# Kernel tuning notes

Measured on AMD Instinct MI355X. Metric: run time of the kernel, lower is better.

Reference implementation:

```python
import jax, jax.numpy as jnp
import numpy as np

N, E, B = 50000, 800000, 64
F0, H, C = 8, 2, 64          # node feat dim, heads, per-head out dim
OBS, MH, NA = 128, 256, 16   # obs dim, mlp hidden, n_actions
NEG_SLOPE = 0.2


def setup_inputs() -> dict:
    key = jax.random.key(0)
    ks = jax.random.split(key, 30)
    p = lambda k, shape: (jax.random.normal(k, shape, dtype=jnp.float32) * 0.1)
    inp = {
        "obs": jax.random.normal(ks[0], (B, OBS), dtype=jnp.float32),
        "node_features": jax.random.normal(ks[1], (N, F0), dtype=jnp.float32),
        "edge_index": jax.random.randint(ks[2], (2, E), 0, N, dtype=jnp.int32),
        "batch": jnp.sort(jax.random.randint(ks[3], (N,), 0, B, dtype=jnp.int32)),
        # GAT layer 0: in=F0 -> heads=H, out=C, concat
        "W0": p(ks[4], (F0, H * C)), "a_src0": p(ks[5], (H, C)), "a_dst0": p(ks[6], (H, C)), "b0": p(ks[7], (H * C,)),
        # GAT layer 1: in=H*C -> heads=H, out=C, concat
        "W1": p(ks[8], (H * C, H * C)), "a_src1": p(ks[9], (H, C)), "a_dst1": p(ks[10], (H, C)), "b1": p(ks[11], (H * C,)),
        # GAT layer 2: in=H*C -> heads=1, out=C, no concat
        "W2": p(ks[12], (H * C, C)), "a_src2": p(ks[13], (1, C)), "a_dst2": p(ks[14], (1, C)), "b2": p(ks[15], (C,)),
        # MLP head: combined = C + OBS
        "Ws1": p(ks[16], (C + OBS, MH)), "bs1": p(ks[17], (MH,)),
        "ln_g": jnp.ones((MH,), jnp.float32), "ln_b": jnp.zeros((MH,), jnp.float32),
        "Ws2": p(ks[18], (MH, MH)), "bs2": p(ks[19], (MH,)),
        "Wa": p(ks[20], (MH, NA)), "ba": p(ks[21], (NA,)),
        "Wc": p(ks[22], (MH, 1)), "bc": p(ks[23], (1,)),
    }
    return inp


def gat_layer(x, src, dst, W, a_src, a_dst, bias, heads, out_dim, concat):
    n = x.shape[0]
    h = (x @ W).reshape(n, heads, out_dim)                     # [N,H,C]
    alpha_s = jnp.einsum("nhc,hc->nh", h, a_src)               # [N,H]
    alpha_d = jnp.einsum("nhc,hc->nh", h, a_dst)
    e = jax.nn.leaky_relu(alpha_s[src] + alpha_d[dst], NEG_SLOPE)  # [E,H]
    # scatter-softmax over incoming edges of each dst node (stable)
    emax = jax.ops.segment_max(e, dst, num_segments=n)
    ex = jnp.exp(e - emax[dst])
    denom = jax.ops.segment_sum(ex, dst, num_segments=n)
    alpha = ex / (denom[dst] + 1e-16)                          # [E,H]
    msg = h[src] * alpha[..., None]                            # [E,H,C]
    out = jax.ops.segment_sum(msg, dst, num_segments=n)        # [N,H,C]
    out = out.reshape(n, heads * out_dim) if concat else out.mean(axis=1)
    return out + bias


def reference(obs, node_features, edge_index, batch,
              W0, a_src0, a_dst0, b0, W1, a_src1, a_dst1, b1,
              W2, a_src2, a_dst2, b2,
              Ws1, bs1, ln_g, ln_b, Ws2, bs2, Wa, ba, Wc, bc):
    n = node_features.shape[0]
    # PyG GATConv default add_self_loops=True
    loop = jnp.arange(n, dtype=edge_index.dtype)
    src = jnp.concatenate([edge_index[0], loop])
    dst = jnp.concatenate([edge_index[1], loop])

    x = node_features
    x = jax.nn.elu(gat_layer(x, src, dst, W0, a_src0, a_dst0, b0, H, C, True))
    x = jax.nn.elu(gat_layer(x, src, dst, W1, a_src1, a_dst1, b1, H, C, True))
    x = gat_layer(x, src, dst, W2, a_src2, a_dst2, b2, 1, C, False)

    # global mean pool over graphs
    counts = jax.ops.segment_sum(jnp.ones((n,), x.dtype), batch, num_segments=B)
    pooled = jax.ops.segment_sum(x, batch, num_segments=B) / jnp.maximum(counts, 1.0)[:, None]

    combined = jnp.concatenate([pooled, obs], axis=-1)         # [B, C+OBS]
    h = combined @ Ws1 + bs1
    mu = h.mean(-1, keepdims=True)
    var = ((h - mu) ** 2).mean(-1, keepdims=True)
    h = (h - mu) / jnp.sqrt(var + 1e-5) * ln_g + ln_b
    h = jax.nn.relu(h)
    h = jax.nn.relu(h @ Ws2 + bs2)
    logits = h @ Wa + ba
    value = (h @ Wc + bc).squeeze(-1)
    return logits, value
```

## Files before the change

### kernel.cpp

```cpp
#include <hip/hip_runtime.h>
#include <math.h>


#define LRELU(x) ((x) > 0.f ? (x) : 0.2f * (x))

typedef short bf16x8 __attribute__((ext_vector_type(8)));
typedef unsigned short u16x8 __attribute__((ext_vector_type(8)));
typedef float f32x4 __attribute__((ext_vector_type(4)));
typedef float f32x2 __attribute__((ext_vector_type(2)));

__device__ __forceinline__ unsigned short f2bf(float f) {
    unsigned int u = __float_as_uint(f);
    u = (u + 0x7fffu + ((u >> 16) & 1u)) >> 16;
    return (unsigned short)u;
}
__device__ __forceinline__ float bf2f(unsigned short u) {
    return __uint_as_float((unsigned int)u << 16);
}
__device__ __forceinline__ unsigned char f2fp8(float f) {
    return (unsigned char)(__builtin_amdgcn_cvt_pk_fp8_f32(f, f, 0, false) & 0xff);
}
__device__ __forceinline__ f32x2 fp8pair(unsigned int u) {
    return __builtin_amdgcn_cvt_pk_f32_fp8(u, false);
}


__global__ __launch_bounds__(256) void hist_t0_kernel(
    const int* __restrict__ dst, int* __restrict__ histT,
    int e, int G1, int NB, int n, int hist_blocks, int t0_blocks, int wp_blocks,
    const float* __restrict__ x, const float* __restrict__ W,
    const float* __restrict__ a_src, const float* __restrict__ a_dst,
    unsigned char* __restrict__ h, float* __restrict__ as_o,
    float* __restrict__ ad_o,
    const float* __restrict__ W1, const float* __restrict__ W2,
    unsigned short* __restrict__ Wf1, unsigned short* __restrict__ Wf2,
    const int* __restrict__ batch, int* __restrict__ gstart, int nGraphs) {
    __shared__ unsigned int hist[512];
    __shared__ float xs[2][8][8];
    const int t = threadIdx.x;
    if ((int)blockIdx.x < hist_blocks) {
        hist[t] = 0;
        hist[t + 256] = 0;
        __syncthreads();
        const int g = blockIdx.x;
#pragma unroll
        for (int jj = 0; jj < 8; jj++) {
            int idx = g * 8192 + jj * 1024 + t * 4;
            int d[4];
            if (idx + 4 <= e) {
                int4 dd = *(const int4*)(dst + idx);
                d[0] = dd.x; d[1] = dd.y; d[2] = dd.z; d[3] = dd.w;
            } else {
#pragma unroll
                for (int q = 0; q < 4; q++) d[q] = (idx + q < e) ? dst[idx + q] : -1;
            }
#pragma unroll
            for (int q = 0; q < 4; q++)
                if (d[q] >= 0) atomicAdd(&hist[d[q] >> 7], 1u);
        }
        __syncthreads();
        if (t < NB) histT[g * NB + t] = (int)hist[t];
        if (t + 256 < NB) histT[g * NB + t + 256] = (int)hist[t + 256];
        return;
    }
    if ((int)blockIdx.x < hist_blocks + t0_blocks) {
        const int bid2 = blockIdx.x - hist_blocks;
        const int tid = t & 127;
        const int half = t >> 7;
        const int node0 = bid2 * 16 + half * 8;

        for (int idx = tid; idx < 64; idx += 128) {
            int ni = idx >> 3, k = idx & 7;
            int ng = node0 + ni;
            xs[half][ni][k] = (ng < n) ? x[(size_t)ng * 8 + k] : 0.f;
        }
        __syncthreads();

        float acc[8];
#pragma unroll
        for (int i = 0; i < 8; i++) acc[i] = 0.f;
#pragma unroll
        for (int k = 0; k < 8; k++) {
            float wk = W[k * 128 + tid];
#pragma unroll
            for (int i = 0; i < 8; i++) acc[i] += xs[half][i][k] * wk;
        }

        const int lane = tid & 63;
        const int head = tid >> 6;
        const int pos = 2 * lane + head;
        const float av = a_src[tid];
        const float dv = a_dst[tid];
#pragma unroll
        for (int i = 0; i < 8; i++) {
            int ng = node0 + i;
            if (ng >= n) break;
            h[(size_t)ng * 128 + pos] = f2fp8(acc[i]);
            float ps = acc[i] * av, pd = acc[i] * dv;
            for (int off = 32; off; off >>= 1) {
                ps += __shfl_xor(ps, off, 64);
                pd += __shfl_xor(pd, off, 64);
            }
            if (lane == 0) {
                as_o[ng * 2 + head] = ps;
                ad_o[ng * 2 + head] = pd;
            }
        }
        return;
    }
    if ((int)blockIdx.x < hist_blocks + t0_blocks + wp_blocks) {
        const int n1 = 8 * 4 * 64;
        const int n2 = 4 * 4 * 64;
        int gid = (blockIdx.x - hist_blocks - t0_blocks) * 256 + t;
        if (gid < n1) {
            int idx = gid;
            int lane = idx & 63, ts = idx >> 6;
            int s = ts & 3, tt = ts >> 2;
            int quad = lane >> 4, cn = lane & 15;
#pragma unroll
            for (int j = 0; j < 8; j++)
                Wf1[idx * 8 + j] = f2bf(W1[(s * 32 + quad * 8 + j) * 128 + tt * 16 + cn]);
        } else if (gid < n1 + n2) {
            int idx = gid - n1;
            int lane = idx & 63, ts = idx >> 6;
            int s = ts & 3, tt = ts >> 2;
            int quad = lane >> 4, cn = lane & 15;
#pragma unroll
            for (int j = 0; j < 8; j++)
                Wf2[idx * 8 + j] = f2bf(W2[(s * 32 + quad * 8 + j) * 64 + tt * 16 + cn]);
        }
        return;
    }
    int gid = (blockIdx.x - hist_blocks - t0_blocks - wp_blocks) * 256 + t;
    if (gid < n) {
        int bi = batch[gid];
        if (gid == 0) {
            for (int g = 0; g <= bi; g++) gstart[g] = 0;
        } else {
            int bp = batch[gid - 1];
            if (bi != bp)
                for (int g = bp + 1; g <= bi; g++) gstart[g] = gid;
        }
        if (gid == n - 1) {
            for (int g = bi + 1; g <= nGraphs; g++) gstart[g] = n;
        }
    }
}


__global__ __launch_bounds__(256) void bucket_scatter_kernel(
    const int* __restrict__ src, const int* __restrict__ dst,
    const int* __restrict__ histT, int* __restrict__ esrc,
    unsigned char* __restrict__ dsub8, int* __restrict__ prefA,
    int e, int G1, int NB) {
    __shared__ int totL[512], scn[256], prefL[512], baseL[512];
    __shared__ unsigned cnt[512];
    const int t = threadIdx.x;
    const int g = blockIdx.x;

    int p0 = 0, tt0 = 0, p1 = 0, tt1 = 0;
    const bool hasHi = (t + 256) < NB;
    for (int g2 = 0; g2 < G1; g2++) {
        int v0 = (t < NB) ? histT[g2 * NB + t] : 0;
        int v1 = hasHi ? histT[g2 * NB + t + 256] : 0;
        if (g2 < g) { p0 += v0; p1 += v1; }
        tt0 += v0; tt1 += v1;
    }
    totL[t] = (t < NB) ? tt0 : 0;
    totL[t + 256] = hasHi ? tt1 : 0;
    __syncthreads();
    int v0 = totL[2 * t], v1 = totL[2 * t + 1];
    int s = v0 + v1;
    scn[t] = s;
    __syncthreads();
    for (int off = 1; off < 256; off <<= 1) {
        int u = (t >= off) ? scn[t - off] : 0;
        __syncthreads();
        scn[t] += u;
        __syncthreads();
    }
    int base2 = scn[t] - s;
    prefL[2 * t] = base2;
    prefL[2 * t + 1] = base2 + v0;
    __syncthreads();
    baseL[t] = prefL[t] + p0;
    baseL[t + 256] = prefL[t + 256] + p1;
    cnt[t] = 0;
    cnt[t + 256] = 0;
    if (g == 0) {
        if (t < NB) prefA[t] = prefL[t];
        if (hasHi) prefA[t + 256] = prefL[t + 256];
        if (t == 0) prefA[NB] = scn[255];
    }
    __syncthreads();

#pragma unroll
    for (int jj = 0; jj < 8; jj++) {
        int idx = g * 8192 + jj * 1024 + t * 4;
        int d[4], sv[4];
        if (idx + 4 <= e) {
            int4 dd = *(const int4*)(dst + idx);
            int4 ss = *(const int4*)(src + idx);
            d[0] = dd.x; d[1] = dd.y; d[2] = dd.z; d[3] = dd.w;
            sv[0] = ss.x; sv[1] = ss.y; sv[2] = ss.z; sv[3] = ss.w;
        } else {
#pragma unroll
            for (int q = 0; q < 4; q++) {
                bool v = idx + q < e;
                d[q] = v ? dst[idx + q] : -1;
                sv[q] = v ? src[idx + q] : 0;
            }
        }
        unsigned r[4];
#pragma unroll
        for (int q = 0; q < 4; q++)
            r[q] = (d[q] >= 0) ? atomicAdd(&cnt[d[q] >> 7], 1u) : 0u;
#pragma unroll
        for (int q = 0; q < 4; q++) {
            if (d[q] >= 0) {
                int pos = baseL[d[q] >> 7] + (int)r[q];
                esrc[pos] = sv[q];
                dsub8[pos] = (unsigned char)(d[q] & 127);
            }
        }
    }
}


__global__ __launch_bounds__(256) void bucket_csr_kernel(
    const int* __restrict__ prefA, const unsigned char* __restrict__ dsub8,
    const int* __restrict__ esrc, int* __restrict__ row_ptr,
    int* __restrict__ col, int n) {
    __shared__ unsigned int cnt[128];
    __shared__ int rp[128];
    const int t = threadIdx.x;
    const int b = blockIdx.x;
    const int bs = prefA[b];
    const int be = prefA[b + 1];
    if (t < 128) cnt[t] = 0;
    __syncthreads();
    for (int i = bs + t; i < be; i += 256) {
        atomicAdd(&cnt[dsub8[i]], 1u);
    }
    __syncthreads();
    int v = 0;
    if (t < 128) { v = (int)cnt[t]; rp[t] = v; }
    __syncthreads();
    for (int off = 1; off < 128; off <<= 1) {
        int u = (t >= off && t < 128) ? rp[t - off] : 0;
        __syncthreads();
        if (t < 128) rp[t] += u;
        __syncthreads();
    }
    if (t < 128) {
        int excl = rp[t] - v;
        int node = b * 128 + t;
        if (node <= n) row_ptr[node] = bs + excl;
        cnt[t] = (unsigned)excl;
    }
    __syncthreads();
    for (int i = bs + t; i < be; i += 256) {
        int sub = dsub8[i];
        unsigned r = atomicAdd(&cnt[sub], 1u);
        col[bs + (int)r] = esrc[i];
    }
}

template <int OUT, int HEADS>
__device__ __forceinline__ int hpos8(int c) {
    return (HEADS == 2) ? (2 * (c & 63) + (c >> 6)) : c;
}


template <int OUT, int HEADS>
__global__ __launch_bounds__(256) void transform_mfma_kernel(
    const unsigned short* __restrict__ xb, const unsigned short* __restrict__ Wf,
    const float* __restrict__ a_src, const float* __restrict__ a_dst,
    unsigned char* __restrict__ h, float* __restrict__ as_o, float* __restrict__ ad_o,
    int n) {
    constexpr int T = OUT / 16, S = 4;
    const int w = threadIdx.x >> 6, lane = threadIdx.x & 63;
    const int node0 = (blockIdx.x * 4 + w) * 16;
    if (node0 >= n) return;
    const int quad = lane >> 4, col = lane & 15;

    const int arow = node0 + col;
    const bool aok = arow < n;
    bf16x8 a[S];
    const unsigned short* xrow = xb + (size_t)arow * 128 + quad * 8;
#pragma unroll
    for (int s = 0; s < S; s++) {
        bf16x8 z = {0, 0, 0, 0, 0, 0, 0, 0};
        a[s] = aok ? *(const bf16x8*)(xrow + s * 32) : z;
    }

    f32x4 acc[T];
#pragma unroll
    for (int t = 0; t < T; t++) acc[t] = (f32x4){0.f, 0.f, 0.f, 0.f};

#pragma unroll
    for (int s = 0; s < S; s++) {
#pragma unroll
        for (int t = 0; t < T; t++) {
            bf16x8 b = *(const bf16x8*)(Wf + ((size_t)(t * S + s) * 64 + lane) * 8);
            acc[t] = __builtin_amdgcn_mfma_f32_16x16x32_bf16(a[s], b, acc[t], 0, 0, 0);
        }
    }

#pragma unroll
    for (int t = 0; t < T; t++) {
        int pos = hpos8<OUT, HEADS>(t * 16 + col);
#pragma unroll
        for (int r = 0; r < 4; r++) {
            int m = node0 + quad * 4 + r;
            if (m < n) h[(size_t)m * OUT + pos] = f2fp8(acc[t][r]);
        }
    }

#pragma unroll
    for (int r = 0; r < 4; r++) {
        float s0 = 0.f, s1 = 0.f, d0 = 0.f, d1 = 0.f;
#pragma unroll
        for (int t = 0; t < T; t++) {
            float av = a_src[t * 16 + col];
            float dv = a_dst[t * 16 + col];
            float v = acc[t][r];
            if (HEADS == 2 && t >= T / 2) { s1 += v * av; d1 += v * dv; }
            else                          { s0 += v * av; d0 += v * dv; }
        }
        for (int off = 8; off; off >>= 1) {
            s0 += __shfl_xor(s0, off, 64);
            d0 += __shfl_xor(d0, off, 64);
            if (HEADS == 2) {
                s1 += __shfl_xor(s1, off, 64);
                d1 += __shfl_xor(d1, off, 64);
            }
        }
        int m = node0 + quad * 4 + r;
        if (m < n) {
            if (HEADS == 2) {
                if (col == 0)      { as_o[m * 2] = s0;     ad_o[m * 2] = d0; }
                else if (col == 1) { as_o[m * 2 + 1] = s1; ad_o[m * 2 + 1] = d1; }
            } else {
                if (col == 0) { as_o[m] = s0; ad_o[m] = d0; }
            }
        }
    }
}


template <int ACT>
__global__ __launch_bounds__(256) void agg2_kernel(
    const int* __restrict__ row_ptr, const int* __restrict__ col,
    const unsigned char* __restrict__ h, const float2* __restrict__ as2,
    const float2* __restrict__ ad2, const float* __restrict__ bias,
    unsigned short* __restrict__ out, int n) {
    __shared__ float w0l[4][2][32], w1l[4][2][32];
    __shared__ unsigned sofl[4][2][32];
    const int w = threadIdx.x >> 6;
    const int lane = threadIdx.x & 63;
    const int half = lane >> 5, l = lane & 31;
    const int node = blockIdx.x * 8 + w * 2 + half;
    const bool active = node < n;

    int beg = 0, deg = 0;
    float2 adv = make_float2(0.f, 0.f);
    float den0 = 0.f, den1 = 0.f;
    float a0 = 0.f, a1 = 0.f, a2 = 0.f, a3 = 0.f;
    if (active) {
        beg = row_ptr[node];
        deg = row_ptr[node + 1] - beg;
        adv = ad2[node];
        float2 avs = as2[node];
        float w0s = __expf(LRELU(avs.x + adv.x));
        float w1s = __expf(LRELU(avs.y + adv.y));
        unsigned us = *(const unsigned*)(h + ((size_t)node << 7) + 4 * l);
        f32x2 p0 = fp8pair(us & 0xffffu);
        f32x2 p1 = fp8pair(us >> 16);
        a0 = w0s * p0.x; a1 = w1s * p0.y;
        a2 = w0s * p1.x; a3 = w1s * p1.y;
        den0 = w0s; den1 = w1s;
    }
    int dmax = deg;
    for (int off = 32; off; off >>= 1) dmax = max(dmax, __shfl_xor(dmax, off, 64));

    for (int base = 0; base < dmax; base += 32) {
        int cnt = deg - base;
        cnt = cnt < 0 ? 0 : (cnt > 32 ? 32 : cnt);
        float w0 = 0.f, w1 = 0.f;
        unsigned so = 0;
        if (l < cnt) {
            int s = col[beg + base + l];
            float2 av = as2[s];
            w0 = __expf(LRELU(av.x + adv.x));
            w1 = __expf(LRELU(av.y + adv.y));
            so = (unsigned)s << 7;
        }
        float t0 = w0, t1 = w1;
        for (int off = 16; off; off >>= 1) {
            t0 += __shfl_xor(t0, off, 64);
            t1 += __shfl_xor(t1, off, 64);
        }
        den0 += t0; den1 += t1;
        w0l[w][half][l] = w0;
        w1l[w][half][l] = w1;
        sofl[w][half][l] = so;

        int jmax = dmax - base;
        jmax = jmax > 32 ? 32 : jmax;
        for (int j = 0; j < jmax; j += 8) {
            unsigned u[8];
#pragma unroll
            for (int k = 0; k < 8; k++) {
                unsigned so_k = sofl[w][half][j + k];
                u[k] = *(const unsigned*)(h + so_k + 4 * l);
            }
            float W0[8], W1[8];
#pragma unroll
            for (int k = 0; k < 8; k++) {
                W0[k] = w0l[w][half][j + k];
                W1[k] = w1l[w][half][j + k];
            }
#pragma unroll
            for (int k = 0; k < 8; k++) {
                f32x2 p0 = fp8pair(u[k] & 0xffffu);
                f32x2 p1 = fp8pair(u[k] >> 16);
                a0 += W0[k] * p0.x; a1 += W1[k] * p0.y;
                a2 += W0[k] * p1.x; a3 += W1[k] * p1.y;
            }
        }
    }

    if (active) {
        float2 bA = *(const float2*)(bias + 2 * l);
        float2 bB = *(const float2*)(bias + 64 + 2 * l);
        float r0 = 1.f / (den0 + 1e-16f), r1 = 1.f / (den1 + 1e-16f);
        float o0 = a0 * r0 + bA.x;
        float o1 = a1 * r1 + bB.x;
        float o2 = a2 * r0 + bA.y;
        float o3 = a3 * r1 + bB.y;
        if (ACT) {
            o0 = o0 > 0.f ? o0 : expm1f(o0);
            o1 = o1 > 0.f ? o1 : expm1f(o1);
            o2 = o2 > 0.f ? o2 : expm1f(o2);
            o3 = o3 > 0.f ? o3 : expm1f(o3);
        }
        unsigned h0 = (unsigned)f2bf(o0) | ((unsigned)f2bf(o2) << 16);
        unsigned h1 = (unsigned)f2bf(o1) | ((unsigned)f2bf(o3) << 16);
        *(unsigned*)(out + (size_t)node * 128 + 2 * l) = h0;
        *(unsigned*)(out + (size_t)node * 128 + 64 + 2 * l) = h1;
    }
}


__global__ __launch_bounds__(256) void agg1_kernel(
    const int* __restrict__ row_ptr, const int* __restrict__ col,
    const unsigned char* __restrict__ h, const float* __restrict__ as1,
    const float* __restrict__ ad1, const float* __restrict__ bias,
    unsigned short* __restrict__ out, int n) {
    __shared__ float wl[4][2][32];
    __shared__ unsigned sofl[4][2][32];
    const int w = threadIdx.x >> 6;
    const int lane = threadIdx.x & 63;
    const int half = lane >> 5, l = lane & 31;
    const int node = blockIdx.x * 8 + w * 2 + half;
    const bool active = node < n;

    int beg = 0, deg = 0;
    float adv = 0.f, den = 0.f, a0 = 0.f, a2 = 0.f;
    if (active) {
        beg = row_ptr[node];
        deg = row_ptr[node + 1] - beg;
        adv = ad1[node];
        float ws = __expf(LRELU(as1[node] + adv));
        unsigned us = *(const unsigned short*)(h + ((size_t)node << 6) + 2 * l);
        f32x2 p = fp8pair(us);
        a0 = ws * p.x;
        a2 = ws * p.y;
        den = ws;
    }
    int dmax = deg;
    for (int off = 32; off; off >>= 1) dmax = max(dmax, __shfl_xor(dmax, off, 64));

    for (int base = 0; base < dmax; base += 32) {
        int cnt = deg - base;
        cnt = cnt < 0 ? 0 : (cnt > 32 ? 32 : cnt);
        float w0 = 0.f;
        unsigned so = 0;
        if (l < cnt) {
            int s = col[beg + base + l];
            w0 = __expf(LRELU(as1[s] + adv));
            so = (unsigned)s << 6;
        }
        float t = w0;
        for (int off = 16; off; off >>= 1) t += __shfl_xor(t, off, 64);
        den += t;
        wl[w][half][l] = w0;
        sofl[w][half][l] = so;

        int jmax = dmax - base;
        jmax = jmax > 32 ? 32 : jmax;
        for (int j = 0; j < jmax; j += 8) {
            unsigned u[8];
#pragma unroll
            for (int k = 0; k < 8; k++) {
                unsigned so_k = sofl[w][half][j + k];
                u[k] = *(const unsigned short*)(h + so_k + 2 * l);
            }
            float W0[8];
#pragma unroll
            for (int k = 0; k < 8; k++) W0[k] = wl[w][half][j + k];
#pragma unroll
            for (int k = 0; k < 8; k++) {
                f32x2 p = fp8pair(u[k]);
                a0 += W0[k] * p.x;
                a2 += W0[k] * p.y;
            }
        }
    }

    if (active) {
        float2 bA = *(const float2*)(bias + 2 * l);
        float r = 1.f / (den + 1e-16f);
        float o0 = a0 * r + bA.x;
        float o2 = a2 * r + bA.y;
        unsigned hv = (unsigned)f2bf(o0) | ((unsigned)f2bf(o2) << 16);
        *(unsigned*)(out + (size_t)node * 64 + 2 * l) = hv;
    }
}


__global__ __launch_bounds__(512) void mlp_kernel(
    const unsigned short* __restrict__ xbuf, const int* __restrict__ gstart,
    const float* __restrict__ obs,
    const float* __restrict__ Ws1, const float* __restrict__ bs1,
    const float* __restrict__ ln_g, const float* __restrict__ ln_b,
    const float* __restrict__ Ws2, const float* __restrict__ bs2,
    const float* __restrict__ Wa, const float* __restrict__ ba,
    const float* __restrict__ Wc, const float* __restrict__ bc,
    float* __restrict__ out_logits, float* __restrict__ out_value) {
    int b = blockIdx.x;
    int t = threadIdx.x;
    __shared__ float comb[192];
    __shared__ float red[512];
    __shared__ float red2[8][64];
    __shared__ float hs[256];

    const int gs = gstart[b];
    const int ge = gstart[b + 1];

    {
        const int w = t >> 6, lane = t & 63;
        const int rg = w * 8 + (lane >> 3);
        const int sub = lane & 7;
        float acc[8];
#pragma unroll
        for (int j = 0; j < 8; j++) acc[j] = 0.f;
        for (int i = gs + rg; i < ge; i += 64) {
            u16x8 v = *(const u16x8*)(xbuf + (size_t)i * 64 + sub * 8);
#pragma unroll
            for (int j = 0; j < 8; j++) acc[j] += bf2f(v[j]);
        }
#pragma unroll
        for (int off = 8; off <= 32; off <<= 1) {
#pragma unroll
            for (int j = 0; j < 8; j++) acc[j] += __shfl_xor(acc[j], off, 64);
        }
        if (lane < 8) {
#pragma unroll
            for (int j = 0; j < 8; j++) red2[w][lane * 8 + j] = acc[j];
        }
    }
    __syncthreads();
    {
        float cdiv = fmaxf((float)(ge - gs), 1.f);
        if (t < 64) {
            float s = 0.f;
#pragma unroll
            for (int w = 0; w < 8; w++) s += red2[w][t];
            comb[t] = s / cdiv;
        } else if (t < 192) {
            comb[t] = obs[b * 128 + (t - 64)];
        }
    }
    __syncthreads();

    const int t256 = t & 255;
    const int khalf = t >> 8;

    {
        float accA = 0.f, accB = 0.f;
        int k0 = khalf * 96;
#pragma unroll 4
        for (int k = k0; k < k0 + 96; k += 2) {
            accA += comb[k] * Ws1[k * 256 + t256];
            accB += comb[k + 1] * Ws1[(k + 1) * 256 + t256];
        }
        red[t] = accA + accB;
    }
    __syncthreads();
    float acc = 0.f;
    if (t < 256) acc = bs1[t] + red[t] + red[t + 256];
    __syncthreads();

    red[t] = (t < 256) ? acc : 0.f;
    __syncthreads();
    for (int off = 128; off; off >>= 1) {
        if (t < off) red[t] += red[t + off];
        __syncthreads();
    }
    float mu = red[0] / 256.f;
    __syncthreads();
    float d = acc - mu;
    red[t] = (t < 256) ? d * d : 0.f;
    __syncthreads();
    for (int off = 128; off; off >>= 1) {
        if (t < off) red[t] += red[t + off];
        __syncthreads();
    }
    float var = red[0] / 256.f;
    if (t < 256) {
        float hn = d * rsqrtf(var + 1e-5f) * ln_g[t] + ln_b[t];
        hs[t] = hn > 0.f ? hn : 0.f;
    }
    __syncthreads();

    {
        float a2A = 0.f, a2B = 0.f;
        int k0 = khalf * 128;
#pragma unroll 4
        for (int k = k0; k < k0 + 128; k += 2) {
            a2A += hs[k] * Ws2[k * 256 + t256];
            a2B += hs[k + 1] * Ws2[(k + 1) * 256 + t256];
        }
        red[t] = a2A + a2B;
    }
    __syncthreads();
    float acc2 = 0.f;
    if (t < 256) {
        acc2 = bs2[t] + red[t] + red[t + 256];
        acc2 = acc2 > 0.f ? acc2 : 0.f;
    }
    __syncthreads();
    if (t < 256) hs[t] = acc2;
    __syncthreads();

    {
        int o = t & 15, ck = t >> 4;
        float p = 0.f;
#pragma unroll
        for (int k = 0; k < 8; k++)
            p += hs[ck * 8 + k] * Wa[(ck * 8 + k) * 16 + o];
        red[t] = p;
    }
    __syncthreads();
    for (int off = 16; off >= 1; off >>= 1) {
        if ((t >> 4) < off) red[t] += red[t + off * 16];
        __syncthreads();
    }
    if (t < 16) out_logits[b * 16 + t] = red[t] + ba[t];
    __syncthreads();

    red[t] = (t < 256) ? hs[t] * Wc[t] : 0.f;
    __syncthreads();
    for (int off = 256; off; off >>= 1) {
        if (t < off) red[t] += red[t + off];
        __syncthreads();
    }
    if (t == 0) out_value[b] = red[0] + bc[0];
}


extern "C" void kernel_launch(void* const* d_in, const int* in_sizes, int n_in,
                              void* d_out, int out_size, void* d_ws, size_t ws_size,
                              hipStream_t stream) {
    const float* obs    = (const float*)d_in[0];
    const float* nf     = (const float*)d_in[1];
    const int*   ei     = (const int*)d_in[2];
    const int*   batch  = (const int*)d_in[3];
    const float* W0     = (const float*)d_in[4];
    const float* a_src0 = (const float*)d_in[5];
    const float* a_dst0 = (const float*)d_in[6];
    const float* b0     = (const float*)d_in[7];
    const float* W1     = (const float*)d_in[8];
    const float* a_src1 = (const float*)d_in[9];
    const float* a_dst1 = (const float*)d_in[10];
    const float* b1     = (const float*)d_in[11];
    const float* W2     = (const float*)d_in[12];
    const float* a_src2 = (const float*)d_in[13];
    const float* a_dst2 = (const float*)d_in[14];
    const float* b2     = (const float*)d_in[15];
    const float* Ws1    = (const float*)d_in[16];
    const float* bs1    = (const float*)d_in[17];
    const float* ln_g   = (const float*)d_in[18];
    const float* ln_b   = (const float*)d_in[19];
    const float* Ws2    = (const float*)d_in[20];
    const float* bs2    = (const float*)d_in[21];
    const float* Wa     = (const float*)d_in[22];
    const float* ba     = (const float*)d_in[23];
    const float* Wc     = (const float*)d_in[24];
    const float* bc     = (const float*)d_in[25];

    const int N = in_sizes[3];
    const int E = in_sizes[2] / 2;
    const int B = in_sizes[0] / 128;
    const int* src = ei;
    const int* dstp = ei + E;

    char* p = (char*)d_ws;
    auto alloc = [&](size_t bytes) -> void* {
        void* r = (void*)p;
        p += (bytes + 255) & ~(size_t)255;
        return r;
    };
    const int G1 = (E + 8191) / 8192;
    const int NB = (N + 127) >> 7;
    int*   row_ptr   = (int*)alloc((size_t)(N + 1) * 4);
    int*   col       = (int*)alloc((size_t)E * 4);
    int*   esrc      = (int*)alloc((size_t)E * 4);
    unsigned char* dsub8 = (unsigned char*)alloc((size_t)E);
    int*   histT     = (int*)alloc((size_t)G1 * NB * 4);
    int*   prefA     = (int*)alloc((size_t)(NB + 1) * 4);
    unsigned char* hbuf = (unsigned char*)alloc((size_t)N * 128);
    unsigned short* xb = (unsigned short*)alloc((size_t)N * 128 * 2);
    unsigned short* xbuf = (unsigned short*)alloc((size_t)N * 64 * 2);
    float* as_       = (float*)alloc((size_t)N * 2 * 4);
    float* ad_       = (float*)alloc((size_t)N * 2 * 4);
    unsigned short* Wf1 = (unsigned short*)alloc((size_t)8 * 4 * 64 * 8 * 2);
    unsigned short* Wf2 = (unsigned short*)alloc((size_t)4 * 4 * 64 * 8 * 2);
    int* gstart      = (int*)alloc((size_t)(B + 1) * 4);

    float* out_logits = (float*)d_out;
    float* out_value  = out_logits + (size_t)B * 16;

    int t0_blocks = (N + 15) / 16;
    int wp_blocks = (8 * 4 * 64 + 4 * 4 * 64 + 255) / 256;
    int gb_blocks = (N + 255) / 256;
    hist_t0_kernel<<<G1 + t0_blocks + wp_blocks + gb_blocks, 256, 0, stream>>>(
        dstp, histT, E, G1, NB, N, G1, t0_blocks, wp_blocks,
        nf, W0, a_src0, a_dst0, hbuf, as_, ad_,
        W1, W2, Wf1, Wf2, batch, gstart, B);

    bucket_scatter_kernel<<<G1, 256, 0, stream>>>(
        src, dstp, histT, esrc, dsub8, prefA, E, G1, NB);
    bucket_csr_kernel<<<NB, 256, 0, stream>>>(
        prefA, dsub8, esrc, row_ptr, col, N);

    agg2_kernel<1><<<(N + 7) / 8, 256, 0, stream>>>(
        row_ptr, col, hbuf, (const float2*)as_, (const float2*)ad_, b0, xb, N);

    transform_mfma_kernel<128, 2><<<(N + 63) / 64, 256, 0, stream>>>(
        xb, Wf1, a_src1, a_dst1, hbuf, as_, ad_, N);
    agg2_kernel<1><<<(N + 7) / 8, 256, 0, stream>>>(
        row_ptr, col, hbuf, (const float2*)as_, (const float2*)ad_, b1, xb, N);

    transform_mfma_kernel<64, 1><<<(N + 63) / 64, 256, 0, stream>>>(
        xb, Wf2, a_src2, a_dst2, hbuf, as_, ad_, N);
    agg1_kernel<<<(N + 7) / 8, 256, 0, stream>>>(
        row_ptr, col, hbuf, as_, ad_, b2, xbuf, N);

    mlp_kernel<<<B, 512, 0, stream>>>(xbuf, gstart, obs, Ws1, bs1, ln_g, ln_b,
                                      Ws2, bs2, Wa, ba, Wc, bc,
                                      out_logits, out_value);
}
```

Baseline: 288.6 us.

## Split bucket scatter chunks across four blocks with prefix recount

Each 8192-edge chunk of the bucket scatter is now handled by four blocks instead of one, each scattering a 2048-edge quarter. To find its write offsets, each block first recounts the destination buckets of the earlier quarters of its chunk using shared-memory atomics. This raises the block count (G1 to 4*G1) to use more of the GPU. The cost is redundant reading and counting of the prefix edges and a longer histogram prefix phase repeated in every block.

Measured after the change: 283.2 us. About the same (-1.8%).

```diff
diff --git a/kernel.cpp b/kernel.cpp
--- a/kernel.cpp
+++ b/kernel.cpp
@@ -156,7 +156,8 @@
     __shared__ int totL[512], scn[256], prefL[512], baseL[512];
     __shared__ unsigned cnt[512];
     const int t = threadIdx.x;
-    const int g = blockIdx.x;
+    const int g = blockIdx.x >> 2;
+    const int q = blockIdx.x & 3;
 
     int p0 = 0, tt0 = 0, p1 = 0, tt1 = 0;
     const bool hasHi = (t + 256) < NB;
@@ -187,16 +188,34 @@
     baseL[t + 256] = prefL[t + 256] + p1;
     cnt[t] = 0;
     cnt[t + 256] = 0;
-    if (g == 0) {
+    if (blockIdx.x == 0) {
         if (t < NB) prefA[t] = prefL[t];
         if (hasHi) prefA[t + 256] = prefL[t + 256];
         if (t == 0) prefA[NB] = scn[255];
     }
     __syncthreads();
 
-#pragma unroll
-    for (int jj = 0; jj < 8; jj++) {
-        int idx = g * 8192 + jj * 1024 + t * 4;
+    const int cbase = g * 8192;
+    const int pre = q * 2048;
+    for (int i = t * 4; i < pre; i += 1024) {
+        int idx = cbase + i;
+        int d[4];
+        if (idx + 4 <= e) {
+            int4 dd = *(const int4*)(dst + idx);
+            d[0] = dd.x; d[1] = dd.y; d[2] = dd.z; d[3] = dd.w;
+        } else {
+#pragma unroll
+            for (int k = 0; k < 4; k++) d[k] = (idx + k < e) ? dst[idx + k] : -1;
+        }
+#pragma unroll
+        for (int k = 0; k < 4; k++)
+            if (d[k] >= 0) atomicAdd(&cnt[d[k] >> 7], 1u);
+    }
+    __syncthreads();
+
+#pragma unroll
+    for (int jj = 0; jj < 2; jj++) {
+        int idx = cbase + pre + jj * 1024 + t * 4;
         int d[4], sv[4];
         if (idx + 4 <= e) {
             int4 dd = *(const int4*)(dst + idx);
@@ -205,22 +224,22 @@
             sv[0] = ss.x; sv[1] = ss.y; sv[2] = ss.z; sv[3] = ss.w;
         } else {
 #pragma unroll
-            for (int q = 0; q < 4; q++) {
-                bool v = idx + q < e;
-                d[q] = v ? dst[idx + q] : -1;
-                sv[q] = v ? src[idx + q] : 0;
+            for (int k = 0; k < 4; k++) {
+                bool v = idx + k < e;
+                d[k] = v ? dst[idx + k] : -1;
+                sv[k] = v ? src[idx + k] : 0;
             }
         }
         unsigned r[4];
 #pragma unroll
-        for (int q = 0; q < 4; q++)
-            r[q] = (d[q] >= 0) ? atomicAdd(&cnt[d[q] >> 7], 1u) : 0u;
-#pragma unroll
-        for (int q = 0; q < 4; q++) {
-            if (d[q] >= 0) {
-                int pos = baseL[d[q] >> 7] + (int)r[q];
-                esrc[pos] = sv[q];
-                dsub8[pos] = (unsigned char)(d[q] & 127);
+        for (int k = 0; k < 4; k++)
+            r[k] = (d[k] >= 0) ? atomicAdd(&cnt[d[k] >> 7], 1u) : 0u;
+#pragma unroll
+        for (int k = 0; k < 4; k++) {
+            if (d[k] >= 0) {
+                int pos = baseL[d[k] >> 7] + (int)r[k];
+                esrc[pos] = sv[k];
+                dsub8[pos] = (unsigned char)(d[k] & 127);
             }
         }
     }
@@ -741,7 +760,7 @@
         nf, W0, a_src0, a_dst0, hbuf, as_, ad_,
         W1, W2, Wf1, Wf2, batch, gstart, B);
 
-    bucket_scatter_kernel<<<G1, 256, 0, stream>>>(
+    bucket_scatter_kernel<<<G1 * 4, 256, 0, stream>>>(
         src, dstp, histT, esrc, dsub8, prefA, E, G1, NB);
     bucket_csr_kernel<<<NB, 256, 0, stream>>>(
         prefA, dsub8, esrc, row_ptr, col, N);
```
